# Performance work log

Measured on AMD Instinct MI355X. Metric: run time of the kernel, lower is better.

The kernel has to match this reference:

```python
import jax, jax.numpy as jnp
import numpy as np

N, E, IN_C, HID, OUT_C = 100000, 1600000, 256, 64, 64
K, ALPHA, LN_EPS = 10, 0.1, 1e-5


def _layernorm(h, gamma, beta):
    mu = jnp.mean(h, axis=-1, keepdims=True)
    var = jnp.var(h, axis=-1, keepdims=True)
    return (h - mu) * jax.lax.rsqrt(var + LN_EPS) * gamma + beta


def _appnp(h, edge_index):
    # gcn_norm with added self-loops (fill value 1), symmetric normalization
    n = h.shape[0]
    sl = jnp.arange(n)
    row = jnp.concatenate([edge_index[0], sl])
    col = jnp.concatenate([edge_index[1], sl])
    w = jnp.ones(row.shape[0], dtype=h.dtype)
    deg = jax.ops.segment_sum(w, col, num_segments=n)
    dinv = jnp.where(deg > 0, jax.lax.rsqrt(deg), 0.0)
    norm = dinv[row] * w * dinv[col]  # [E+N]
    h0 = h
    for _ in range(K):
        msg = norm[:, None] * h[row]                       # gather [E+N, HID]
        agg = jax.ops.segment_sum(msg, col, num_segments=n)  # scatter-add
        h = (1.0 - ALPHA) * agg + ALPHA * h0
    return h


def setup_inputs() -> dict:
    key = jax.random.key(0)
    ks = jax.random.split(key, 8)
    x = jax.random.normal(ks[0], (N, IN_C), dtype=jnp.float32)
    edge_index = jax.random.randint(ks[1], (2, E), 0, N, dtype=jnp.int64)
    W1 = jax.random.normal(ks[2], (IN_C, HID), dtype=jnp.float32) / np.sqrt(IN_C)
    b1 = jnp.zeros((HID,), dtype=jnp.float32)
    g1 = jnp.ones((HID,), dtype=jnp.float32)
    be1 = jnp.zeros((HID,), dtype=jnp.float32)
    g2 = jnp.ones((HID,), dtype=jnp.float32)
    be2 = jnp.zeros((HID,), dtype=jnp.float32)
    W2 = jax.random.normal(ks[3], (HID, OUT_C), dtype=jnp.float32) / np.sqrt(HID)
    b2 = jnp.zeros((OUT_C,), dtype=jnp.float32)
    return {"x": x, "edge_index": edge_index, "W1": W1, "b1": b1,
            "g1": g1, "be1": be1, "g2": g2, "be2": be2, "W2": W2, "b2": b2}


def reference(x, edge_index, W1, b1, g1, be1, g2, be2, W2, b2):
    h = jax.nn.gelu(x @ W1 + b1, approximate=False)   # Linear + exact GELU (torch default)
    h = _layernorm(h, g1, be1)
    h = jax.nn.gelu(_appnp(h, edge_index), approximate=False)
    h = _layernorm(h, g2, be2)
    # dropout inactive in eval mode
    return h @ W2 + b2
```

## Files before the change

### kernel.cpp

```cpp
#include <hip/hip_runtime.h>
#include <math.h>

#define HID 64
#define INC 256
#define LN_EPS 1e-5f
#define ALPHA 0.1f
#define NBKT 256
#define BCAP 12288

typedef unsigned short ushort_t;
typedef unsigned int uint_t;
using short8v = __attribute__((ext_vector_type(8))) short;
using float4v = __attribute__((ext_vector_type(4))) float;

__device__ __forceinline__ float gelu_exact(float x) {
    return 0.5f * x * (1.0f + erff(x * 0.70710678118654752f));
}

__device__ __forceinline__ float wave_sum64(float v) {
#pragma unroll
    for (int m = 1; m < 64; m <<= 1) v += __shfl_xor(v, m, 64);
    return v;
}

__device__ __forceinline__ ushort_t f2bf(float f) {
    uint_t u = __float_as_uint(f);
    return (ushort_t)((u + 0x7fffu + ((u >> 16) & 1u)) >> 16);
}
__device__ __forceinline__ float bf_lo(uint_t v) { return __uint_as_float(v << 16); }
__device__ __forceinline__ float bf_hi(uint_t v) { return __uint_as_float(v & 0xffff0000u); }

__device__ __forceinline__ void split_bf(float f, ushort_t& hi, ushort_t& lo) {
    uint_t ub = __float_as_uint(f);
    uint_t h = (ub + 0x7fffu + ((ub >> 16) & 1u)) >> 16;
    hi = (ushort_t)h;
    float fl = f - __uint_as_float(h << 16);
    uint_t lb = __float_as_uint(fl);
    lo = (ushort_t)((lb + 0x7fffu + ((lb >> 16) & 1u)) >> 16);
}

__global__ __launch_bounds__(256) void k_prepW(const float* __restrict__ W1,
                                               ushort_t* __restrict__ whi,
                                               ushort_t* __restrict__ wlo) {
    int e = blockIdx.x * 256 + threadIdx.x;
    int col = e & 63, k = e >> 6;
    float f = W1[(size_t)k * HID + col];
    ushort_t hi, lo;
    split_bf(f, hi, lo);
    int idx = col * 256 + (((k >> 3) ^ (col & 7)) << 3) + (k & 7);
    whi[idx] = hi;
    wlo[idx] = lo;
}

__global__ __launch_bounds__(256) void k_prepW2(const float* __restrict__ W2,
                                                ushort_t* __restrict__ whi,
                                                ushort_t* __restrict__ wlo) {
    int e = blockIdx.x * 256 + threadIdx.x;
    int col = e & 63, k = e >> 6;
    float f = W2[(size_t)k * HID + col];
    ushort_t hi, lo;
    split_bf(f, hi, lo);
    int idx = col * 64 + (((k >> 3) ^ (col & 7)) << 3) + (k & 7);
    whi[idx] = hi;
    wlo[idx] = lo;
}

__global__ __launch_bounds__(256) void k_bin(const int* __restrict__ ei,
                                             int* __restrict__ bcur,
                                             uint_t* __restrict__ binned, int E) {
    __shared__ int hist[NBKT];
    __shared__ int base[NBKT];
    const int t = threadIdx.x;
    const int c0 = blockIdx.x * 4096;
    hist[t] = 0;
    __syncthreads();
#pragma unroll
    for (int i = 0; i < 16; ++i) {
        int e = c0 + i * 256 + t;
        if (e < E) atomicAdd(&hist[ei[E + e] >> 9], 1);
    }
    __syncthreads();
    {
        int h = hist[t];
        base[t] = (h > 0) ? atomicAdd(&bcur[t], h) : 0;
        hist[t] = 0;
    }
    __syncthreads();
#pragma unroll
    for (int i = 0; i < 16; ++i) {
        int e = c0 + i * 256 + t;
        if (e < E) {
            int src = ei[e];
            int dst = ei[E + e];
            int b = dst >> 9;
            int r = atomicAdd(&hist[b], 1);
            int pos = base[b] + r;
            if (pos >= BCAP) pos = BCAP - 1;
            binned[(size_t)b * BCAP + pos] = (uint_t)src | ((uint_t)(dst & 511) << 20);
        }
    }
}

__global__ __launch_bounds__(256) void k_bktscan(const int* __restrict__ bcur,
                                                 int* __restrict__ bbase,
                                                 int* __restrict__ rowstart, int N, int E) {
    __shared__ int s[256];
    const int t = threadIdx.x;
    const int v = bcur[t];
    s[t] = v;
    __syncthreads();
#pragma unroll
    for (int off = 1; off < 256; off <<= 1) {
        int add = (t >= off) ? s[t - off] : 0;
        __syncthreads();
        s[t] += add;
        __syncthreads();
    }
    bbase[t] = s[t] - v;
    if (t == 0) rowstart[N] = E;
}

__global__ __launch_bounds__(256) void k_csr(const uint_t* __restrict__ binned,
                                             const int* __restrict__ bcur,
                                             const int* __restrict__ bbase,
                                             int* __restrict__ csr,
                                             int* __restrict__ cnt,
                                             float* __restrict__ dinv,
                                             int* __restrict__ rowstart, int N) {
    __shared__ int cl[512];
    __shared__ int off[512];
    __shared__ int ps[256];
    const int b = blockIdx.x, t = threadIdx.x;
    const int nE = bcur[b];
    const int gbase = bbase[b];
    const uint_t* be = binned + (size_t)b * BCAP;
    cl[t] = 0;
    cl[t + 256] = 0;
    __syncthreads();
    for (int i = t; i < nE; i += 256) atomicAdd(&cl[be[i] >> 20], 1);
    __syncthreads();
    const int pa = cl[2 * t], pb_ = cl[2 * t + 1];
    const int p = pa + pb_;
    ps[t] = p;
    __syncthreads();
#pragma unroll
    for (int o = 1; o < 256; o <<= 1) {
        int add = (t >= o) ? ps[t - o] : 0;
        __syncthreads();
        ps[t] += add;
        __syncthreads();
    }
    const int pbase = ps[t] - p;
    off[2 * t] = pbase;
    off[2 * t + 1] = pbase + pa;
    __syncthreads();
    const int n0 = b * 512;
    for (int i = t; i < 512; i += 256) {
        int g = n0 + i;
        if (g < N) {
            int c = cl[i];
            cnt[g] = c;
            dinv[g] = rsqrtf((float)(c + 1));
            rowstart[g] = gbase + off[i];
        }
    }
    __syncthreads();
    for (int i = t; i < nE; i += 256) {
        uint_t rec = be[i];
        int ln = rec >> 20;
        int r = atomicAdd(&off[ln], 1);
        csr[gbase + r] = (int)(rec & 0xFFFFFu);
    }
}

__global__ __launch_bounds__(256) void k_gemm1ln(const float* __restrict__ x,
                                                 const ushort_t* __restrict__ whi,
                                                 const ushort_t* __restrict__ wlo,
                                                 const float* __restrict__ b1,
                                                 const float* __restrict__ g1,
                                                 const float* __restrict__ be1,
                                                 const float* __restrict__ dinv,
                                                 ushort_t* __restrict__ u0, int N) {
    __shared__ ushort_t Wh[16384];
    __shared__ ushort_t Wl[16384];
    const int t = threadIdx.x;
    {
        const uint4* s1 = (const uint4*)whi;
        uint4* d1 = (uint4*)Wh;
        for (int i = t; i < 2048; i += 256) d1[i] = s1[i];
        const uint4* s2 = (const uint4*)wlo;
        uint4* d2 = (uint4*)Wl;
        for (int i = t; i < 2048; i += 256) d2[i] = s2[i];
    }
    __syncthreads();

    const int lane = t & 63, w = t >> 6;
    const int l15 = lane & 15, lg = lane >> 4;
    const int row0 = blockIdx.x * 64 + w * 16;
    int rowc = row0 + l15;
    if (rowc > N - 1) rowc = N - 1;
    const float* xr = x + (size_t)rowc * INC + lg * 8;

    float4 A0 = *(const float4*)(xr);
    float4 A1 = *(const float4*)(xr + 4);
    float4v acc[4];
#pragma unroll
    for (int i = 0; i < 4; ++i) acc[i] = (float4v){0.f, 0.f, 0.f, 0.f};

    union U8 { short8v v; ushort_t u[8]; };

#pragma unroll
    for (int t8 = 0; t8 < 8; ++t8) {
        float4 P0, P1;
        if (t8 < 7) {
            P0 = *(const float4*)(xr + (t8 + 1) * 32);
            P1 = *(const float4*)(xr + (t8 + 1) * 32 + 4);
        }
        U8 ahi, alo;
        {
            const float af[8] = {A0.x, A0.y, A0.z, A0.w, A1.x, A1.y, A1.z, A1.w};
#pragma unroll
            for (int j = 0; j < 8; ++j) split_bf(af[j], ahi.u[j], alo.u[j]);
        }
#pragma unroll
        for (int ct = 0; ct < 4; ++ct) {
            const int col = ct * 16 + l15;
            const int kb = t8 * 4 + lg;
            const int idx = col * 256 + ((kb ^ (col & 7)) << 3);
            short8v bhi = *(const short8v*)&Wh[idx];
            short8v blo = *(const short8v*)&Wl[idx];
            acc[ct] = __builtin_amdgcn_mfma_f32_16x16x32_bf16(ahi.v, bhi, acc[ct], 0, 0, 0);
            acc[ct] = __builtin_amdgcn_mfma_f32_16x16x32_bf16(ahi.v, blo, acc[ct], 0, 0, 0);
            acc[ct] = __builtin_amdgcn_mfma_f32_16x16x32_bf16(alo.v, bhi, acc[ct], 0, 0, 0);
        }
        if (t8 < 7) { A0 = P0; A1 = P1; }
    }

    float b1c[4], g1c[4], bec[4];
#pragma unroll
    for (int ct = 0; ct < 4; ++ct) {
        const int col = ct * 16 + l15;
        b1c[ct] = b1[col];
        g1c[ct] = g1[col];
        bec[ct] = be1[col];
    }
    float gv[4][4];
#pragma unroll
    for (int ct = 0; ct < 4; ++ct)
#pragma unroll
        for (int r = 0; r < 4; ++r) gv[ct][r] = gelu_exact(acc[ct][r] + b1c[ct]);

    float mu[4], rsv[4];
#pragma unroll
    for (int r = 0; r < 4; ++r) {
        float p = gv[0][r] + gv[1][r] + gv[2][r] + gv[3][r];
        p += __shfl_xor(p, 1, 64);
        p += __shfl_xor(p, 2, 64);
        p += __shfl_xor(p, 4, 64);
        p += __shfl_xor(p, 8, 64);
        mu[r] = p * (1.0f / 64.0f);
        float d0 = gv[0][r] - mu[r], d1 = gv[1][r] - mu[r];
        float d2 = gv[2][r] - mu[r], d3 = gv[3][r] - mu[r];
        float p2 = d0 * d0 + d1 * d1 + d2 * d2 + d3 * d3;
        p2 += __shfl_xor(p2, 1, 64);
        p2 += __shfl_xor(p2, 2, 64);
        p2 += __shfl_xor(p2, 4, 64);
        p2 += __shfl_xor(p2, 8, 64);
        rsv[r] = rsqrtf(p2 * (1.0f / 64.0f) + LN_EPS);
    }
#pragma unroll
    for (int r = 0; r < 4; ++r) {
        const int row = row0 + lg * 4 + r;
        if (row < N) {
            const float di = dinv[row];
#pragma unroll
            for (int ct = 0; ct < 4; ++ct) {
                const float ln = (gv[ct][r] - mu[r]) * rsv[r] * g1c[ct] + bec[ct];
                u0[(size_t)row * HID + ct * 16 + l15] = f2bf(di * ln);
            }
        }
    }
}

__global__ __launch_bounds__(256) void k_prop(const ushort_t* __restrict__ uin,
                                              const ushort_t* __restrict__ u0,
                                              ushort_t* __restrict__ uout,
                                              const int* __restrict__ csr,
                                              const int* __restrict__ rowstart,
                                              const float* __restrict__ dinv, int N) {
    const int t = threadIdx.x;
    const int lane = t & 63;
    const int q = lane >> 4, fl = lane & 15;
    const int node = blockIdx.x * 4 + (t >> 6);
    if (node >= N) return;
    const uint2* U = (const uint2*)uin;
    const int s0 = rowstart[node];
    const int e1 = rowstart[node + 1];
    float a0 = 0.f, a1 = 0.f, a2 = 0.f, a3 = 0.f;
    for (int e = s0; e < e1; e += 16) {
        int idx[4];
        bool ok[4];
#pragma unroll
        for (int b = 0; b < 4; ++b) {
            const int i = e + b * 4 + q;
            ok[b] = i < e1;
            idx[b] = csr[ok[b] ? i : s0];
        }
        uint2 v[4];
#pragma unroll
        for (int b = 0; b < 4; ++b) v[b] = U[(size_t)idx[b] * 16 + fl];
#pragma unroll
        for (int b = 0; b < 4; ++b) {
            const float f = ok[b] ? 1.0f : 0.0f;
            a0 = fmaf(f, bf_lo(v[b].x), a0);
            a1 = fmaf(f, bf_hi(v[b].x), a1);
            a2 = fmaf(f, bf_lo(v[b].y), a2);
            a3 = fmaf(f, bf_hi(v[b].y), a3);
        }
    }
    a0 += __shfl_xor(a0, 16, 64); a0 += __shfl_xor(a0, 32, 64);
    a1 += __shfl_xor(a1, 16, 64); a1 += __shfl_xor(a1, 32, 64);
    a2 += __shfl_xor(a2, 16, 64); a2 += __shfl_xor(a2, 32, 64);
    a3 += __shfl_xor(a3, 16, 64); a3 += __shfl_xor(a3, 32, 64);
    if (lane < 16) {
        const uint2 ud = U[(size_t)node * 16 + fl];
        const uint2 uz = ((const uint2*)u0)[(size_t)node * 16 + fl];
        const float di = dinv[node];
        const float c = (1.0f - ALPHA) * di * di;
        const float r0 = c * (a0 + bf_lo(ud.x)) + ALPHA * bf_lo(uz.x);
        const float r1 = c * (a1 + bf_hi(ud.x)) + ALPHA * bf_hi(uz.x);
        const float r2 = c * (a2 + bf_lo(ud.y)) + ALPHA * bf_lo(uz.y);
        const float r3 = c * (a3 + bf_hi(ud.y)) + ALPHA * bf_hi(uz.y);
        uint2 o;
        o.x = (uint_t)f2bf(r0) | ((uint_t)f2bf(r1) << 16);
        o.y = (uint_t)f2bf(r2) | ((uint_t)f2bf(r3) << 16);
        ((uint2*)uout)[(size_t)node * 16 + fl] = o;
    }
}

__global__ __launch_bounds__(256) void k_final(const ushort_t* __restrict__ u,
                                               const int* __restrict__ cnt,
                                               const float* __restrict__ g2,
                                               const float* __restrict__ be2,
                                               const ushort_t* __restrict__ w2hi,
                                               const ushort_t* __restrict__ w2lo,
                                               const float* __restrict__ b2,
                                               float* __restrict__ out, int N) {
    __shared__ ushort_t Wh[4096];
    __shared__ ushort_t Wl[4096];
    const int t = threadIdx.x;
    {
        const uint4* s1 = (const uint4*)w2hi;
        uint4* d1 = (uint4*)Wh;
        for (int i = t; i < 512; i += 256) d1[i] = s1[i];
        const uint4* s2 = (const uint4*)w2lo;
        uint4* d2 = (uint4*)Wl;
        for (int i = t; i < 512; i += 256) d2[i] = s2[i];
    }
    __syncthreads();

    const int lane = t & 63, w = t >> 6;
    const int l15 = lane & 15, lg = lane >> 4;
    const int row0 = blockIdx.x * 64 + w * 16;
    if (row0 >= N) return;
    int rowc = row0 + l15;
    if (rowc > N - 1) rowc = N - 1;

    const uint4 uva = *(const uint4*)(u + (size_t)rowc * HID + lg * 8);
    const uint4 uvb = *(const uint4*)(u + (size_t)rowc * HID + 32 + lg * 8);
    const float sc = sqrtf((float)(cnt[rowc] + 1));

    float v[16];
    {
        const uint_t ua_[4] = {uva.x, uva.y, uva.z, uva.w};
        const uint_t ub_[4] = {uvb.x, uvb.y, uvb.z, uvb.w};
#pragma unroll
        for (int j = 0; j < 4; ++j) {
            v[2 * j] = gelu_exact(bf_lo(ua_[j]) * sc);
            v[2 * j + 1] = gelu_exact(bf_hi(ua_[j]) * sc);
            v[8 + 2 * j] = gelu_exact(bf_lo(ub_[j]) * sc);
            v[8 + 2 * j + 1] = gelu_exact(bf_hi(ub_[j]) * sc);
        }
    }
    float s = 0.f;
#pragma unroll
    for (int j = 0; j < 16; ++j) s += v[j];
    s += __shfl_xor(s, 16, 64);
    s += __shfl_xor(s, 32, 64);
    const float mu = s * (1.0f / 64.0f);
    float sq = 0.f;
#pragma unroll
    for (int j = 0; j < 16; ++j) {
        v[j] -= mu;
        sq += v[j] * v[j];
    }
    sq += __shfl_xor(sq, 16, 64);
    sq += __shfl_xor(sq, 32, 64);
    const float rs = rsqrtf(sq * (1.0f / 64.0f) + LN_EPS);

    union U8 { short8v v; ushort_t u[8]; };
    U8 a0, a1;
#pragma unroll
    for (int j = 0; j < 8; ++j) {
        const int ka = lg * 8 + j;
        const int kb = 32 + lg * 8 + j;
        a0.u[j] = f2bf(v[j] * rs * g2[ka] + be2[ka]);
        a1.u[j] = f2bf(v[8 + j] * rs * g2[kb] + be2[kb]);
    }

    float4v acc[4];
#pragma unroll
    for (int i = 0; i < 4; ++i) acc[i] = (float4v){0.f, 0.f, 0.f, 0.f};
#pragma unroll
    for (int ct = 0; ct < 4; ++ct) {
        const int col = ct * 16 + l15;
        const int i0 = col * 64 + ((lg ^ (col & 7)) << 3);
        const int i1 = col * 64 + (((4 + lg) ^ (col & 7)) << 3);
        short8v b0h = *(const short8v*)&Wh[i0];
        short8v b0l = *(const short8v*)&Wl[i0];
        short8v b1h = *(const short8v*)&Wh[i1];
        short8v b1l = *(const short8v*)&Wl[i1];
        acc[ct] = __builtin_amdgcn_mfma_f32_16x16x32_bf16(a0.v, b0h, acc[ct], 0, 0, 0);
        acc[ct] = __builtin_amdgcn_mfma_f32_16x16x32_bf16(a0.v, b0l, acc[ct], 0, 0, 0);
        acc[ct] = __builtin_amdgcn_mfma_f32_16x16x32_bf16(a1.v, b1h, acc[ct], 0, 0, 0);
        acc[ct] = __builtin_amdgcn_mfma_f32_16x16x32_bf16(a1.v, b1l, acc[ct], 0, 0, 0);
    }

#pragma unroll
    for (int ct = 0; ct < 4; ++ct) {
        const float bb = b2[ct * 16 + l15];
#pragma unroll
        for (int r = 0; r < 4; ++r) {
            const int row = row0 + lg * 4 + r;
            if (row < N) out[(size_t)row * HID + ct * 16 + l15] = acc[ct][r] + bb;
        }
    }
}

extern "C" void kernel_launch(void* const* d_in, const int* in_sizes, int n_in,
                              void* d_out, int out_size, void* d_ws, size_t ws_size,
                              hipStream_t stream) {
    const float* x   = (const float*)d_in[0];
    const int*   ei  = (const int*)d_in[1];
    const float* W1  = (const float*)d_in[2];
    const float* b1  = (const float*)d_in[3];
    const float* g1  = (const float*)d_in[4];
    const float* be1 = (const float*)d_in[5];
    const float* g2  = (const float*)d_in[6];
    const float* be2 = (const float*)d_in[7];
    const float* W2  = (const float*)d_in[8];
    const float* b2  = (const float*)d_in[9];
    float* out = (float*)d_out;

    const int N = in_sizes[0] / INC;
    const int E = in_sizes[1] / 2;

    char* ws = (char*)d_ws;
    size_t o = 0;
    auto alloc = [&](size_t bytes) { size_t r = o; o += (bytes + 255) & ~(size_t)255; return r; };
    ushort_t* u0 = (ushort_t*)(ws + alloc((size_t)N * HID * 2));
    ushort_t* ua = (ushort_t*)(ws + alloc((size_t)N * HID * 2));
    ushort_t* ub = (ushort_t*)(ws + alloc((size_t)N * HID * 2));
    float* dinv     = (float*)(ws + alloc((size_t)N * 4));
    int*   cnt      = (int*)(ws + alloc((size_t)N * 4));
    int*   rowstart = (int*)(ws + alloc((size_t)(N + 1) * 4));
    int*   bcur     = (int*)(ws + alloc(NBKT * 4));
    int*   bbase    = (int*)(ws + alloc(NBKT * 4));
    ushort_t* whi   = (ushort_t*)(ws + alloc(16384 * 2));
    ushort_t* wlo   = (ushort_t*)(ws + alloc(16384 * 2));
    ushort_t* w2hi  = (ushort_t*)(ws + alloc(4096 * 2));
    ushort_t* w2lo  = (ushort_t*)(ws + alloc(4096 * 2));
    uint_t* binned  = (uint_t*)(ws + alloc((size_t)NBKT * BCAP * 4));
    int*   csr      = (int*)(ws + alloc((size_t)E * 4));

    const int nbkt = (N + 511) / 512;

    hipMemsetAsync(bcur, 0, NBKT * 4, stream);
    k_prepW<<<64, 256, 0, stream>>>(W1, whi, wlo);
    k_prepW2<<<16, 256, 0, stream>>>(W2, w2hi, w2lo);
    k_bin<<<(E + 4095) / 4096, 256, 0, stream>>>(ei, bcur, binned, E);
    k_bktscan<<<1, 256, 0, stream>>>(bcur, bbase, rowstart, N, E);
    k_csr<<<nbkt, 256, 0, stream>>>(binned, bcur, bbase, csr, cnt, dinv, rowstart, N);
    k_gemm1ln<<<(N + 63) / 64, 256, 0, stream>>>(x, whi, wlo, b1, g1, be1, dinv, u0, N);

    ushort_t* bufs[2] = {ua, ub};
    const ushort_t* pin = u0;
    for (int k = 0; k < 10; ++k) {
        ushort_t* pout = bufs[k & 1];
        k_prop<<<(N + 3) / 4, 256, 0, stream>>>(pin, u0, pout, csr, rowstart, dinv, N);
        pin = pout;
    }
    k_final<<<(N + 63) / 64, 256, 0, stream>>>(pin, cnt, g2, be2, w2hi, w2lo, b2, out, N);
}
```

Before: 527.4 us.

## Pad CSR rows to multiples of four with a zero sentinel node for vector gathers

CSR construction is split into two passes: the first counts per-node degrees and pads each row length up to a multiple of four, and the second scatters edges and fills the padding with a sentinel index pointing at an extra all-zero feature row. The propagation kernel then loads four neighbor indices at once as an int4 and sums their features without per-edge bounds masks. The aim is to cut index-load and predication overhead across the ten propagation passes. Separately, the GEMM1 kernel drops its shared-memory staging of W1 in favour of direct global loads of an unswizzled layout, and preloads the whole x row segment up front. This costs an extra kernel launch, padded CSR storage, extra memsets, and a heavier register and cache load in the GEMM.

```diff
diff --git a/kernel.cpp b/kernel.cpp
--- a/kernel.cpp
+++ b/kernel.cpp
@@ -47,9 +47,8 @@
     float f = W1[(size_t)k * HID + col];
     ushort_t hi, lo;
     split_bf(f, hi, lo);
-    int idx = col * 256 + (((k >> 3) ^ (col & 7)) << 3) + (k & 7);
-    whi[idx] = hi;
-    wlo[idx] = lo;
+    whi[col * 256 + k] = hi;
+    wlo[col * 256 + k] = lo;
 }
 
 __global__ __launch_bounds__(256) void k_prepW2(const float* __restrict__ W2,
@@ -101,12 +100,55 @@
     }
 }
 
-__global__ __launch_bounds__(256) void k_bktscan(const int* __restrict__ bcur,
+__global__ __launch_bounds__(256) void k_csrA(const uint_t* __restrict__ binned,
+                                              const int* __restrict__ bcur,
+                                              int* __restrict__ cnt,
+                                              float* __restrict__ dinv,
+                                              int* __restrict__ offl,
+                                              int* __restrict__ bpad, int N) {
+    __shared__ int cl[512];
+    __shared__ int ps[256];
+    const int b = blockIdx.x, t = threadIdx.x;
+    const int nE = bcur[b];
+    const uint_t* be = binned + (size_t)b * BCAP;
+    cl[t] = 0;
+    cl[t + 256] = 0;
+    __syncthreads();
+    for (int i = t; i < nE; i += 256) atomicAdd(&cl[be[i] >> 20], 1);
+    __syncthreads();
+    const int ca = cl[2 * t], cb = cl[2 * t + 1];
+    const int p4a = (ca + 3) & ~3, p4b = (cb + 3) & ~3;
+    const int p = p4a + p4b;
+    ps[t] = p;
+    __syncthreads();
+#pragma unroll
+    for (int o = 1; o < 256; o <<= 1) {
+        int add = (t >= o) ? ps[t - o] : 0;
+        __syncthreads();
+        ps[t] += add;
+        __syncthreads();
+    }
+    const int pbase = ps[t] - p;
+    const int g0 = b * 512 + 2 * t;
+    if (g0 < N) {
+        cnt[g0] = ca;
+        dinv[g0] = rsqrtf((float)(ca + 1));
+        offl[g0] = pbase;
+    }
+    if (g0 + 1 < N) {
+        cnt[g0 + 1] = cb;
+        dinv[g0 + 1] = rsqrtf((float)(cb + 1));
+        offl[g0 + 1] = pbase + p4a;
+    }
+    if (t == 255) bpad[b] = ps[255];
+}
+
+__global__ __launch_bounds__(256) void k_bktscan(const int* __restrict__ bpad,
                                                  int* __restrict__ bbase,
-                                                 int* __restrict__ rowstart, int N, int E) {
+                                                 int* __restrict__ rowstart, int N) {
     __shared__ int s[256];
     const int t = threadIdx.x;
-    const int v = bcur[t];
+    const int v = bpad[t];
     s[t] = v;
     __syncthreads();
 #pragma unroll
@@ -117,59 +159,45 @@
         __syncthreads();
     }
     bbase[t] = s[t] - v;
-    if (t == 0) rowstart[N] = E;
-}
-
-__global__ __launch_bounds__(256) void k_csr(const uint_t* __restrict__ binned,
-                                             const int* __restrict__ bcur,
-                                             const int* __restrict__ bbase,
-                                             int* __restrict__ csr,
-                                             int* __restrict__ cnt,
-                                             float* __restrict__ dinv,
-                                             int* __restrict__ rowstart, int N) {
-    __shared__ int cl[512];
-    __shared__ int off[512];
-    __shared__ int ps[256];
+    if (t == 255) rowstart[N] = s[255];
+}
+
+__global__ __launch_bounds__(256) void k_csrB(const uint_t* __restrict__ binned,
+                                              const int* __restrict__ bcur,
+                                              const int* __restrict__ bbase,
+                                              const int* __restrict__ offl,
+                                              const int* __restrict__ cnt,
+                                              int* __restrict__ csr,
+                                              int* __restrict__ rowstart, int N) {
+    __shared__ int st[512];
+    __shared__ int cur[512];
     const int b = blockIdx.x, t = threadIdx.x;
     const int nE = bcur[b];
-    const int gbase = bbase[b];
+    const int gb = bbase[b];
     const uint_t* be = binned + (size_t)b * BCAP;
-    cl[t] = 0;
-    cl[t + 256] = 0;
-    __syncthreads();
-    for (int i = t; i < nE; i += 256) atomicAdd(&cl[be[i] >> 20], 1);
-    __syncthreads();
-    const int pa = cl[2 * t], pb_ = cl[2 * t + 1];
-    const int p = pa + pb_;
-    ps[t] = p;
-    __syncthreads();
-#pragma unroll
-    for (int o = 1; o < 256; o <<= 1) {
-        int add = (t >= o) ? ps[t - o] : 0;
-        __syncthreads();
-        ps[t] += add;
-        __syncthreads();
-    }
-    const int pbase = ps[t] - p;
-    off[2 * t] = pbase;
-    off[2 * t + 1] = pbase + pa;
-    __syncthreads();
     const int n0 = b * 512;
     for (int i = t; i < 512; i += 256) {
         int g = n0 + i;
-        if (g < N) {
-            int c = cl[i];
-            cnt[g] = c;
-            dinv[g] = rsqrtf((float)(c + 1));
-            rowstart[g] = gbase + off[i];
-        }
+        int s = (g < N) ? gb + offl[g] : 0;
+        st[i] = s;
+        cur[i] = s;
+        if (g < N) rowstart[g] = s;
     }
     __syncthreads();
     for (int i = t; i < nE; i += 256) {
         uint_t rec = be[i];
         int ln = rec >> 20;
-        int r = atomicAdd(&off[ln], 1);
-        csr[gbase + r] = (int)(rec & 0xFFFFFu);
+        int r = atomicAdd(&cur[ln], 1);
+        csr[r] = (int)(rec & 0xFFFFFu);
+    }
+    __syncthreads();
+    for (int i = t; i < 512; i += 256) {
+        int g = n0 + i;
+        if (g < N) {
+            int c = cnt[g];
+            int end = st[i] + ((c + 3) & ~3);
+            for (int j = st[i] + c; j < end; ++j) csr[j] = N;
+        }
     }
 }
 
@@ -181,19 +209,7 @@
                                                  const float* __restrict__ be1,
                                                  const float* __restrict__ dinv,
                                                  ushort_t* __restrict__ u0, int N) {
-    __shared__ ushort_t Wh[16384];
-    __shared__ ushort_t Wl[16384];
     const int t = threadIdx.x;
-    {
-        const uint4* s1 = (const uint4*)whi;
-        uint4* d1 = (uint4*)Wh;
-        for (int i = t; i < 2048; i += 256) d1[i] = s1[i];
-        const uint4* s2 = (const uint4*)wlo;
-        uint4* d2 = (uint4*)Wl;
-        for (int i = t; i < 2048; i += 256) d2[i] = s2[i];
-    }
-    __syncthreads();
-
     const int lane = t & 63, w = t >> 6;
     const int l15 = lane & 15, lg = lane >> 4;
     const int row0 = blockIdx.x * 64 + w * 16;
@@ -201,8 +217,13 @@
     if (rowc > N - 1) rowc = N - 1;
     const float* xr = x + (size_t)rowc * INC + lg * 8;
 
-    float4 A0 = *(const float4*)(xr);
-    float4 A1 = *(const float4*)(xr + 4);
+    float4 ax[16];
+#pragma unroll
+    for (int i = 0; i < 8; ++i) {
+        ax[2 * i] = *(const float4*)(xr + i * 32);
+        ax[2 * i + 1] = *(const float4*)(xr + i * 32 + 4);
+    }
+
     float4v acc[4];
 #pragma unroll
     for (int i = 0; i < 4; ++i) acc[i] = (float4v){0.f, 0.f, 0.f, 0.f};
@@ -211,29 +232,24 @@
 
 #pragma unroll
     for (int t8 = 0; t8 < 8; ++t8) {
-        float4 P0, P1;
-        if (t8 < 7) {
-            P0 = *(const float4*)(xr + (t8 + 1) * 32);
-            P1 = *(const float4*)(xr + (t8 + 1) * 32 + 4);
-        }
         U8 ahi, alo;
         {
-            const float af[8] = {A0.x, A0.y, A0.z, A0.w, A1.x, A1.y, A1.z, A1.w};
+            const float af[8] = {ax[2 * t8].x, ax[2 * t8].y, ax[2 * t8].z, ax[2 * t8].w,
+                                 ax[2 * t8 + 1].x, ax[2 * t8 + 1].y, ax[2 * t8 + 1].z,
+                                 ax[2 * t8 + 1].w};
 #pragma unroll
             for (int j = 0; j < 8; ++j) split_bf(af[j], ahi.u[j], alo.u[j]);
         }
+        const int kb = t8 * 4 + lg;
 #pragma unroll
         for (int ct = 0; ct < 4; ++ct) {
             const int col = ct * 16 + l15;
-            const int kb = t8 * 4 + lg;
-            const int idx = col * 256 + ((kb ^ (col & 7)) << 3);
-            short8v bhi = *(const short8v*)&Wh[idx];
-            short8v blo = *(const short8v*)&Wl[idx];
+            const short8v bhi = *(const short8v*)(whi + col * 256 + kb * 8);
+            const short8v blo = *(const short8v*)(wlo + col * 256 + kb * 8);
             acc[ct] = __builtin_amdgcn_mfma_f32_16x16x32_bf16(ahi.v, bhi, acc[ct], 0, 0, 0);
             acc[ct] = __builtin_amdgcn_mfma_f32_16x16x32_bf16(ahi.v, blo, acc[ct], 0, 0, 0);
             acc[ct] = __builtin_amdgcn_mfma_f32_16x16x32_bf16(alo.v, bhi, acc[ct], 0, 0, 0);
         }
-        if (t8 < 7) { A0 = P0; A1 = P1; }
     }
 
     float b1c[4], g1c[4], bec[4];
@@ -298,25 +314,17 @@
     const int e1 = rowstart[node + 1];
     float a0 = 0.f, a1 = 0.f, a2 = 0.f, a3 = 0.f;
     for (int e = s0; e < e1; e += 16) {
-        int idx[4];
-        bool ok[4];
-#pragma unroll
-        for (int b = 0; b < 4; ++b) {
-            const int i = e + b * 4 + q;
-            ok[b] = i < e1;
-            idx[b] = csr[ok[b] ? i : s0];
-        }
-        uint2 v[4];
-#pragma unroll
-        for (int b = 0; b < 4; ++b) v[b] = U[(size_t)idx[b] * 16 + fl];
-#pragma unroll
-        for (int b = 0; b < 4; ++b) {
-            const float f = ok[b] ? 1.0f : 0.0f;
-            a0 = fmaf(f, bf_lo(v[b].x), a0);
-            a1 = fmaf(f, bf_hi(v[b].x), a1);
-            a2 = fmaf(f, bf_lo(v[b].y), a2);
-            a3 = fmaf(f, bf_hi(v[b].y), a3);
-        }
+        const int ge = e + 4 * q;
+        int4 id = make_int4(N, N, N, N);
+        if (ge < e1) id = *(const int4*)(csr + ge);
+        const uint2 v0 = U[(size_t)id.x * 16 + fl];
+        const uint2 v1 = U[(size_t)id.y * 16 + fl];
+        const uint2 v2 = U[(size_t)id.z * 16 + fl];
+        const uint2 v3 = U[(size_t)id.w * 16 + fl];
+        a0 += bf_lo(v0.x) + bf_lo(v1.x) + bf_lo(v2.x) + bf_lo(v3.x);
+        a1 += bf_hi(v0.x) + bf_hi(v1.x) + bf_hi(v2.x) + bf_hi(v3.x);
+        a2 += bf_lo(v0.y) + bf_lo(v1.y) + bf_lo(v2.y) + bf_lo(v3.y);
+        a3 += bf_hi(v0.y) + bf_hi(v1.y) + bf_hi(v2.y) + bf_hi(v3.y);
     }
     a0 += __shfl_xor(a0, 16, 64); a0 += __shfl_xor(a0, 32, 64);
     a1 += __shfl_xor(a1, 16, 64); a1 += __shfl_xor(a1, 32, 64);
@@ -458,29 +466,37 @@
     char* ws = (char*)d_ws;
     size_t o = 0;
     auto alloc = [&](size_t bytes) { size_t r = o; o += (bytes + 255) & ~(size_t)255; return r; };
-    ushort_t* u0 = (ushort_t*)(ws + alloc((size_t)N * HID * 2));
-    ushort_t* ua = (ushort_t*)(ws + alloc((size_t)N * HID * 2));
-    ushort_t* ub = (ushort_t*)(ws + alloc((size_t)N * HID * 2));
+    ushort_t* u0 = (ushort_t*)(ws + alloc((size_t)(N + 1) * HID * 2));
+    ushort_t* ua = (ushort_t*)(ws + alloc((size_t)(N + 1) * HID * 2));
+    ushort_t* ub = (ushort_t*)(ws + alloc((size_t)(N + 1) * HID * 2));
     float* dinv     = (float*)(ws + alloc((size_t)N * 4));
     int*   cnt      = (int*)(ws + alloc((size_t)N * 4));
+    int*   offl     = (int*)(ws + alloc((size_t)N * 4));
     int*   rowstart = (int*)(ws + alloc((size_t)(N + 1) * 4));
     int*   bcur     = (int*)(ws + alloc(NBKT * 4));
+    int*   bpad     = (int*)(ws + alloc(NBKT * 4));
     int*   bbase    = (int*)(ws + alloc(NBKT * 4));
     ushort_t* whi   = (ushort_t*)(ws + alloc(16384 * 2));
     ushort_t* wlo   = (ushort_t*)(ws + alloc(16384 * 2));
     ushort_t* w2hi  = (ushort_t*)(ws + alloc(4096 * 2));
     ushort_t* w2lo  = (ushort_t*)(ws + alloc(4096 * 2));
     uint_t* binned  = (uint_t*)(ws + alloc((size_t)NBKT * BCAP * 4));
-    int*   csr      = (int*)(ws + alloc((size_t)E * 4));
+    int*   csr      = (int*)(ws + alloc((size_t)(E + 3 * (size_t)N + 256) * 4));
 
     const int nbkt = (N + 511) / 512;
 
     hipMemsetAsync(bcur, 0, NBKT * 4, stream);
+    hipMemsetAsync(bpad, 0, NBKT * 4, stream);
+    hipMemsetAsync(u0 + (size_t)N * HID, 0, HID * 2, stream);
+    hipMemsetAsync(ua + (size_t)N * HID, 0, HID * 2, stream);
+    hipMemsetAsync(ub + (size_t)N * HID, 0, HID * 2, stream);
+
     k_prepW<<<64, 256, 0, stream>>>(W1, whi, wlo);
     k_prepW2<<<16, 256, 0, stream>>>(W2, w2hi, w2lo);
     k_bin<<<(E + 4095) / 4096, 256, 0, stream>>>(ei, bcur, binned, E);
-    k_bktscan<<<1, 256, 0, stream>>>(bcur, bbase, rowstart, N, E);
-    k_csr<<<nbkt, 256, 0, stream>>>(binned, bcur, bbase, csr, cnt, dinv, rowstart, N);
+    k_csrA<<<nbkt, 256, 0, stream>>>(binned, bcur, cnt, dinv, offl, bpad, N);
+    k_bktscan<<<1, 256, 0, stream>>>(bpad, bbase, rowstart, N);
+    k_csrB<<<nbkt, 256, 0, stream>>>(binned, bcur, bbase, offl, cnt, csr, rowstart, N);
     k_gemm1ln<<<(N + 63) / 64, 256, 0, stream>>>(x, whi, wlo, b1, g1, be1, dinv, u0, N);
 
     ushort_t* bufs[2] = {ua, ub};
```

Measured after the change: 564.9 us. 7.1% more time.
